# Optimization experiments

Measured on AMD Instinct MI355X. Metric: run time of the kernel, lower is better.

## Reference

```python
import jax, jax.numpy as jnp
import numpy as np

H = W = 240

def setup_inputs() -> dict:
    key = jax.random.key(0)
    k1, k2, k3 = jax.random.split(key, 3)
    B = 256
    T2_Gen = jax.random.normal(k1, (B, 1, H, W), dtype=jnp.float32)
    underT2_K = jax.random.normal(k2, (B, 2, H, W), dtype=jnp.float32)
    # k-space sampling mask (soft in [0,1); original uses a fixed undersampling mask)
    A = jax.random.uniform(k3, (H, W), dtype=jnp.float32)
    return {"T2_Gen": T2_Gen, "underT2_K": underT2_K, "A": A}

def reference(T2_Gen, underT2_K, A):
    # x2: [B, H, W]
    x2 = T2_Gen.reshape(-1, H, W)
    # batched 2D FFT over the last two axes (replaces the per-slice numpy loop)
    x2_k = jnp.fft.fft2(x2)  # complex64
    # undersampled k-space as complex: real = channel 0, imag = channel 1
    y_k = underT2_K[:, 0, :, :] + 1j * underT2_K[:, 1, :, :]
    z_k = (1.0 - A) * x2_k + y_k
    z = jnp.abs(jnp.fft.ifft2(z_k))  # [B, H, W] real
    return z.reshape(-1, 1, H, W)
```

## Files before the change

kernel.cpp:

```cpp
#include <hip/hip_runtime.h>
#include <hip/hip_fp16.h>
#include <math.h>

#define HW 240
#define PITCH 242
#define IMG_PIX (HW*HW)
#define NB 15
#define NBA 8
#define TILE_ELEMS (240*16)
#define CHA 4
#define CHC 3

__device__ __forceinline__ float2 cmul(float2 a, float2 b){
    return make_float2(a.x*b.x - a.y*b.y, a.x*b.y + a.y*b.x);
}
__device__ __forceinline__ float2 cadd(float2 a, float2 b){
    return make_float2(a.x+b.x, a.y+b.y);
}
__device__ __forceinline__ float2 csub(float2 a, float2 b){
    return make_float2(a.x-b.x, a.y-b.y);
}
__device__ __forceinline__ __half2 f2h(float2 a){ return __floats2half2_rn(a.x, a.y); }
__device__ __forceinline__ float2 h2f(__half2 h){ return make_float2(__low2float(h), __high2float(h)); }

__device__ __forceinline__ void wave_fence(){ __builtin_amdgcn_wave_barrier(); }

__device__ __forceinline__ void lds_barrier(){
    asm volatile("s_waitcnt lgkmcnt(0)" ::: "memory");
    __builtin_amdgcn_s_barrier();
    asm volatile("" ::: "memory");
}

template<int SIGN>
__device__ __forceinline__ void dft15(const float2* x, float2* X){
    const float S = (float)SIGN;
    const float s3 = 0.8660254037844387f;
    float2 y[5][3];
    #pragma unroll
    for (int n2 = 0; n2 < 5; ++n2){
        float2 a0 = x[n2], a1 = x[5+n2], a2 = x[10+n2];
        float2 t = cadd(a1, a2);
        float2 u = csub(a1, a2);
        float2 m = make_float2(a0.x - 0.5f*t.x, a0.y - 0.5f*t.y);
        float sx = S * s3;
        float2 s = make_float2(-sx*u.y, sx*u.x);
        y[n2][0] = cadd(a0, t);
        y[n2][1] = cadd(m, s);
        y[n2][2] = csub(m, s);
    }
    const float C15[9] = {1.f, 0.9135454576426009f, 0.6691306063588582f, 0.30901699437494745f,
                          -0.10452846326765346f, -0.5f, -0.8090169943749475f,
                          -0.9781476007338057f, -0.9781476007338057f};
    const float S15[9] = {0.f, 0.4067366430758004f, 0.7431448254773942f, 0.9510565162951535f,
                          0.9945218953682733f, 0.8660254037844387f, 0.5877852522924731f,
                          0.20791169081775931f, -0.20791169081775931f};
    #pragma unroll
    for (int n2 = 1; n2 < 5; ++n2){
        #pragma unroll
        for (int k1 = 1; k1 < 3; ++k1){
            const int e = n2*k1;
            y[n2][k1] = cmul(y[n2][k1], make_float2(C15[e], S*S15[e]));
        }
    }
    const float c1 = 0.30901699437494745f, s1 = 0.9510565162951535f;
    const float c2 = -0.8090169943749475f, s2 = 0.5877852522924731f;
    #pragma unroll
    for (int k1 = 0; k1 < 3; ++k1){
        float2 x0 = y[0][k1], x1 = y[1][k1], x2 = y[2][k1], x3 = y[3][k1], x4 = y[4][k1];
        float2 t1 = cadd(x1, x4), t3 = csub(x1, x4);
        float2 t2 = cadd(x2, x3), t4 = csub(x2, x3);
        X[k1] = make_float2(x0.x + t1.x + t2.x, x0.y + t1.y + t2.y);
        float2 u1 = make_float2(x0.x + c1*t1.x + c2*t2.x, x0.y + c1*t1.y + c2*t2.y);
        float2 u2 = make_float2(x0.x + c2*t1.x + c1*t2.x, x0.y + c2*t1.y + c1*t2.y);
        float2 v1 = make_float2(S*(s1*t3.x + s2*t4.x), S*(s1*t3.y + s2*t4.y));
        float2 v2 = make_float2(S*(s2*t3.x - s1*t4.x), S*(s2*t3.y - s1*t4.y));
        X[k1+3]  = make_float2(u1.x - v1.y, u1.y + v1.x);
        X[k1+12] = make_float2(u1.x + v1.y, u1.y - v1.x);
        X[k1+6]  = make_float2(u2.x - v2.y, u2.y + v2.x);
        X[k1+9]  = make_float2(u2.x + v2.y, u2.y - v2.x);
    }
}

template<int SIGN>
__device__ __forceinline__ void dft16(const float2* x, float2* X){
    const float S = (float)SIGN;
    float2 y[4][4];
    #pragma unroll
    for (int n2 = 0; n2 < 4; ++n2){
        float2 a0 = x[n2], a1 = x[4+n2], a2 = x[8+n2], a3 = x[12+n2];
        float2 t0 = cadd(a0,a2), t1 = csub(a0,a2);
        float2 t2 = cadd(a1,a3), t3 = csub(a1,a3);
        float2 it3 = make_float2(-S*t3.y, S*t3.x);
        y[n2][0] = cadd(t0,t2);
        y[n2][2] = csub(t0,t2);
        y[n2][1] = cadd(t1,it3);
        y[n2][3] = csub(t1,it3);
    }
    const float C16[10] = {1.f, 0.9238795325112867f, 0.7071067811865476f, 0.3826834323650898f,
                           0.f, -0.3826834323650898f, -0.7071067811865476f, -0.9238795325112867f,
                           -1.f, -0.9238795325112867f};
    const float S16[10] = {0.f, 0.3826834323650898f, 0.7071067811865476f, 0.9238795325112867f,
                           1.f, 0.9238795325112867f, 0.7071067811865476f, 0.3826834323650898f,
                           0.f, -0.3826834323650898f};
    #pragma unroll
    for (int n2 = 1; n2 < 4; ++n2){
        #pragma unroll
        for (int k1 = 1; k1 < 4; ++k1){
            const int e = n2*k1;
            y[n2][k1] = cmul(y[n2][k1], make_float2(C16[e], S*S16[e]));
        }
    }
    #pragma unroll
    for (int k1 = 0; k1 < 4; ++k1){
        float2 a0 = y[0][k1], a1 = y[1][k1], a2 = y[2][k1], a3 = y[3][k1];
        float2 t0 = cadd(a0,a2), t1 = csub(a0,a2);
        float2 t2 = cadd(a1,a3), t3 = csub(a1,a3);
        float2 it3 = make_float2(-S*t3.y, S*t3.x);
        X[k1]    = cadd(t0,t2);
        X[k1+8]  = csub(t0,t2);
        X[k1+4]  = cadd(t1,it3);
        X[k1+12] = csub(t1,it3);
    }
}

template<int SIGN>
__device__ __forceinline__ void fft240_core(float2 (*sm)[PITCH], float2* v,
                                            float2* XX, int rl, int b){
    const float TWOPI = 6.28318530717958647692f;
    wave_fence();
    float2 Y[15];
    dft15<SIGN>(v, Y);
    float2 step, tw = make_float2(1.0f, 0.0f);
    {
        float ang = (float)SIGN * TWOPI * (float)b * (1.0f/240.0f);
        __sincosf(ang, &step.y, &step.x);
    }
    #pragma unroll
    for (int d = 0; d < 15; ++d){
        sm[rl][b*15 + d] = cmul(Y[d], tw);
        tw = cmul(tw, step);
    }
    wave_fence();
    float2 Z[16];
    if (b < 15){
        #pragma unroll
        for (int bb = 0; bb < 16; ++bb) Z[bb] = sm[rl][bb*15 + b];
    }
    wave_fence();
    if (b < 15) dft16<SIGN>(Z, XX);
}

template<int SIGN>
__device__ __forceinline__ void fft240(float2 (*sm)[PITCH], float2* v, int rl, int b){
    float2 XX[16];
    fft240_core<SIGN>(sm, v, XX, rl, b);
    if (b < 15){
        #pragma unroll
        for (int m = 0; m < 16; ++m) sm[rl][15*m + b] = XX[m];
    }
    wave_fence();
}

__global__ __launch_bounds__(256) void passA_rowfft(const float* __restrict__ x,
                                                    __half2* __restrict__ out){
    __shared__ __align__(16) float2 sm[15][PITCH];
    int g = blockIdx.x;
    int tid = threadIdx.x, rl = tid >> 4, b = tid & 15;
    if (tid >= 240) return;
    float2 v[15];
    {
        int c = g*CHA; int img = c / NBA, h0 = (c % NBA) * 30;
        const float* r0 = x + (size_t)img * IMG_PIX + (size_t)(h0 + 2*rl) * HW;
        #pragma unroll
        for (int a = 0; a < 15; ++a)
            v[a] = make_float2(r0[16*a + b], r0[HW + 16*a + b]);
    }
    for (int t = 0; t < CHA; ++t){
        int c = g*CHA + t; int img = c / NBA, h0 = (c % NBA) * 30;
        float2 nv[15];
        if (t+1 < CHA){
            int c2 = c + 1; int img2 = c2 / NBA, h02 = (c2 % NBA) * 30;
            const float* r0 = x + (size_t)img2 * IMG_PIX + (size_t)(h02 + 2*rl) * HW;
            #pragma unroll
            for (int a = 0; a < 15; ++a)
                nv[a] = make_float2(r0[16*a + b], r0[HW + 16*a + b]);
        }
        asm volatile("" ::: "memory");
        fft240<-1>(sm, v, rl, b);
        #pragma unroll
        for (int kb = 0; kb < NB; ++kb){
            int k = kb*16 + b;
            int km = k ? 240 - k : 0;
            float2 P = sm[rl][k], Q = sm[rl][km];
            float2 Xa = make_float2(0.5f*(P.x + Q.x), 0.5f*(P.y - Q.y));
            float2 Xb = make_float2(0.5f*(P.y + Q.y), 0.5f*(Q.x - P.x));
            size_t o = ((size_t)(img*NB + kb)*HW + (h0 + 2*rl))*16 + b;
            out[o]      = f2h(Xa);
            out[o + 16] = f2h(Xb);
        }
        if (t+1 < CHA){
            #pragma unroll
            for (int a = 0; a < 15; ++a) v[a] = nv[a];
        }
    }
}

__global__ __launch_bounds__(256) void passB_col_dc_icol(__half2* __restrict__ io,
                                                         const float* __restrict__ under,
                                                         const float* __restrict__ Am){
    __shared__ __align__(16) float2 sm[16][PITCH];
    int g = blockIdx.x, img = g / NB, s = g % NB, kw0 = s * 16;
    int tid = threadIdx.x, rl = tid >> 4, b = tid & 15;
    __half2* chunk = io + (size_t)(img*NB + s) * TILE_ELEMS;

    if (tid < 240){
        #pragma unroll
        for (int jj = 0; jj < 4; ++jj){
            int k = jj*240 + tid;
            float4 raw = *(const float4*)(chunk + 4*k);
            const __half2* hp = (const __half2*)&raw;
            int col = k >> 2;
            int r0 = (4*k) & 15;
            #pragma unroll
            for (int i = 0; i < 4; ++i) sm[r0 + i][col] = h2f(hp[i]);
        }
    }
    const float* y0 = under + (size_t)img * (2*IMG_PIX);
    float y0r[15], y1r[15];
    #pragma unroll
    for (int j = 0; j < 15; ++j){
        size_t p = (size_t)(j*16 + rl) * HW + kw0 + b;
        y0r[j] = y0[p];
        y1r[j] = y0[IMG_PIX + p];
    }
    asm volatile("" ::: "memory");
    lds_barrier();
    float2 v[15];
    #pragma unroll
    for (int a = 0; a < 15; ++a) v[a] = sm[rl][16*a + b];
    float2 XX[16];
    fft240_core<-1>(sm, v, XX, rl, b);
    if (b < 15){
        #pragma unroll
        for (int m = 0; m < 16; ++m) sm[rl][15*m + b] = XX[m];
    }
    lds_barrier();
    #pragma unroll
    for (int j = 0; j < 15; ++j){
        int kh = j*16 + rl;
        size_t p = (size_t)kh * HW + kw0 + b;
        float sc = 1.0f - Am[p];
        float2 X = sm[b][kh];
        sm[b][kh] = make_float2(sc * X.x + y0r[j], sc * X.y + y1r[j]);
    }
    lds_barrier();
    float2 v2[15];
    #pragma unroll
    for (int a = 0; a < 15; ++a) v2[a] = sm[rl][16*a + b];
    float2 ZZ[16];
    fft240_core<+1>(sm, v2, ZZ, rl, b);
    const float inv240 = 1.0f / 240.0f;
    if (b < 15){
        #pragma unroll
        for (int m = 0; m < 16; ++m)
            chunk[(size_t)(15*m + b)*16 + rl] =
                f2h(make_float2(ZZ[m].x*inv240, ZZ[m].y*inv240));
    }
}

__global__ __launch_bounds__(256) void passC_irow_abs(const __half2* __restrict__ in,
                                                      float* __restrict__ outp){
    __shared__ __align__(16) float2 sm[16][PITCH];
    int g = blockIdx.x;
    int tid = threadIdx.x, rl = tid >> 4, b = tid & 15;
    float2 v[15];
    {
        int c = g*CHC; int img = c / NB, h0 = (c % NB) * 16;
        #pragma unroll
        for (int a = 0; a < 15; ++a)
            v[a] = h2f(in[((size_t)(img*NB + a)*HW + h0 + rl)*16 + b]);
    }
    const float inv240 = 1.0f / 240.0f;
    for (int t = 0; t < CHC; ++t){
        int c = g*CHC + t; int img = c / NB, h0 = (c % NB) * 16;
        float2 nv[15];
        if (t+1 < CHC){
            int c2 = c + 1; int img2 = c2 / NB, h02 = (c2 % NB) * 16;
            #pragma unroll
            for (int a = 0; a < 15; ++a)
                nv[a] = h2f(in[((size_t)(img2*NB + a)*HW + h02 + rl)*16 + b]);
        }
        asm volatile("" ::: "memory");
        float2 XX[16];
        fft240_core<+1>(sm, v, XX, rl, b);
        float* dst = outp + (size_t)img * IMG_PIX + (size_t)(h0 + rl) * HW;
        if (b < 15){
            #pragma unroll
            for (int m = 0; m < 16; ++m){
                float2 X = XX[m];
                dst[15*m + b] = sqrtf(X.x*X.x + X.y*X.y) * inv240;
            }
        }
        if (t+1 < CHC){
            #pragma unroll
            for (int a = 0; a < 15; ++a) v[a] = nv[a];
        }
    }
}

extern "C" void kernel_launch(void* const* d_in, const int* in_sizes, int n_in,
                              void* d_out, int out_size, void* d_ws, size_t ws_size,
                              hipStream_t stream){
    const float* T2   = (const float*)d_in[0];
    const float* U    = (const float*)d_in[1];
    const float* Am   = (const float*)d_in[2];
    float* out        = (float*)d_out;

    const int B = 256;
    __half2* i1 = (__half2*)d_ws;

    dim3 block(256);
    passA_rowfft     <<<dim3(B * NBA / CHA), block, 0, stream>>>(T2, i1);
    passB_col_dc_icol<<<dim3(B * NB),        block, 0, stream>>>(i1, U, Am);
    passC_irow_abs   <<<dim3(B * NB / CHC),  block, 0, stream>>>(i1, out);
}
```

Measured before the change: 294.2 us.

## Re-tile intermediate layout so row-FFT writes and column-FFT reads coalesce

Pass A now handles one 16-row strip per block with 128 threads and stages its half-precision spectrum in LDS, so each block writes whole 16-wide tiles with vector stores. Those tiles are laid out so pass B can read its column input directly into registers without an LDS transpose. Pass B now stages its inverse-column result in LDS and writes it back with vector stores in the layout pass C expects. The cross-chunk prefetch and register buffering of the measurement data are dropped, which may expose more load latency.

Measured after the change: 274.1 us. 6.8% less time.

```diff
diff --git a/kernel.cpp b/kernel.cpp
--- a/kernel.cpp
+++ b/kernel.cpp
@@ -6,9 +6,7 @@
 #define PITCH 242
 #define IMG_PIX (HW*HW)
 #define NB 15
-#define NBA 8
 #define TILE_ELEMS (240*16)
-#define CHA 4
 #define CHC 3
 
 __device__ __forceinline__ float2 cmul(float2 a, float2 b){
@@ -161,46 +159,43 @@
     wave_fence();
 }
 
-__global__ __launch_bounds__(256) void passA_rowfft(const float* __restrict__ x,
+
+__global__ __launch_bounds__(128) void passA_rowfft(const float* __restrict__ x,
                                                     __half2* __restrict__ out){
-    __shared__ __align__(16) float2 sm[15][PITCH];
-    int g = blockIdx.x;
+    __shared__ __align__(16) float2 smbuf[8*PITCH];
+    float2 (*sm)[PITCH] = (float2(*)[PITCH])smbuf;
+    __half2* Lh = (__half2*)smbuf;
+    int g = blockIdx.x, img = g / NB, Ag = g % NB, h0 = Ag * 16;
     int tid = threadIdx.x, rl = tid >> 4, b = tid & 15;
-    if (tid >= 240) return;
+    const float* r0 = x + (size_t)img * IMG_PIX + (size_t)(h0 + 2*rl) * HW;
     float2 v[15];
-    {
-        int c = g*CHA; int img = c / NBA, h0 = (c % NBA) * 30;
-        const float* r0 = x + (size_t)img * IMG_PIX + (size_t)(h0 + 2*rl) * HW;
-        #pragma unroll
-        for (int a = 0; a < 15; ++a)
-            v[a] = make_float2(r0[16*a + b], r0[HW + 16*a + b]);
-    }
-    for (int t = 0; t < CHA; ++t){
-        int c = g*CHA + t; int img = c / NBA, h0 = (c % NBA) * 30;
-        float2 nv[15];
-        if (t+1 < CHA){
-            int c2 = c + 1; int img2 = c2 / NBA, h02 = (c2 % NBA) * 30;
-            const float* r0 = x + (size_t)img2 * IMG_PIX + (size_t)(h02 + 2*rl) * HW;
-            #pragma unroll
-            for (int a = 0; a < 15; ++a)
-                nv[a] = make_float2(r0[16*a + b], r0[HW + 16*a + b]);
-        }
-        asm volatile("" ::: "memory");
-        fft240<-1>(sm, v, rl, b);
-        #pragma unroll
-        for (int kb = 0; kb < NB; ++kb){
-            int k = kb*16 + b;
-            int km = k ? 240 - k : 0;
-            float2 P = sm[rl][k], Q = sm[rl][km];
-            float2 Xa = make_float2(0.5f*(P.x + Q.x), 0.5f*(P.y - Q.y));
-            float2 Xb = make_float2(0.5f*(P.y + Q.y), 0.5f*(Q.x - P.x));
-            size_t o = ((size_t)(img*NB + kb)*HW + (h0 + 2*rl))*16 + b;
-            out[o]      = f2h(Xa);
-            out[o + 16] = f2h(Xb);
-        }
-        if (t+1 < CHA){
-            #pragma unroll
-            for (int a = 0; a < 15; ++a) v[a] = nv[a];
+    #pragma unroll
+    for (int a = 0; a < 15; ++a)
+        v[a] = make_float2(r0[16*a + b], r0[HW + 16*a + b]);
+    fft240<-1>(sm, v, rl, b);
+    __half2 xa[15], xb[15];
+    #pragma unroll
+    for (int kb = 0; kb < NB; ++kb){
+        int k = kb*16 + b;
+        int km = k ? 240 - k : 0;
+        float2 P = sm[rl][k], Q = sm[rl][km];
+        xa[kb] = f2h(make_float2(0.5f*(P.x + Q.x), 0.5f*(P.y - Q.y)));
+        xb[kb] = f2h(make_float2(0.5f*(P.y + Q.y), 0.5f*(Q.x - P.x)));
+    }
+    lds_barrier();
+    #pragma unroll
+    for (int kb = 0; kb < NB; ++kb){
+        Lh[kb*256 + b*16 + 2*rl]     = xa[kb];
+        Lh[kb*256 + b*16 + 2*rl + 1] = xb[kb];
+    }
+    lds_barrier();
+    float4* gout = (float4*)out;
+    #pragma unroll
+    for (int i = 0; i < 8; ++i){
+        int u = i*128 + tid;
+        if (u < 960){
+            int seg = u >> 6, e = u & 63;
+            gout[((size_t)(img*NB + seg)*NB + Ag)*64 + e] = ((float4*)Lh)[u];
         }
     }
 }
@@ -213,31 +208,11 @@
     int tid = threadIdx.x, rl = tid >> 4, b = tid & 15;
     __half2* chunk = io + (size_t)(img*NB + s) * TILE_ELEMS;
 
-    if (tid < 240){
-        #pragma unroll
-        for (int jj = 0; jj < 4; ++jj){
-            int k = jj*240 + tid;
-            float4 raw = *(const float4*)(chunk + 4*k);
-            const __half2* hp = (const __half2*)&raw;
-            int col = k >> 2;
-            int r0 = (4*k) & 15;
-            #pragma unroll
-            for (int i = 0; i < 4; ++i) sm[r0 + i][col] = h2f(hp[i]);
-        }
-    }
-    const float* y0 = under + (size_t)img * (2*IMG_PIX);
-    float y0r[15], y1r[15];
-    #pragma unroll
-    for (int j = 0; j < 15; ++j){
-        size_t p = (size_t)(j*16 + rl) * HW + kw0 + b;
-        y0r[j] = y0[p];
-        y1r[j] = y0[IMG_PIX + p];
-    }
-    asm volatile("" ::: "memory");
-    lds_barrier();
     float2 v[15];
     #pragma unroll
-    for (int a = 0; a < 15; ++a) v[a] = sm[rl][16*a + b];
+    for (int a = 0; a < 15; ++a)
+        v[a] = h2f(chunk[a*256 + rl*16 + b]);
+
     float2 XX[16];
     fft240_core<-1>(sm, v, XX, rl, b);
     if (b < 15){
@@ -245,13 +220,14 @@
         for (int m = 0; m < 16; ++m) sm[rl][15*m + b] = XX[m];
     }
     lds_barrier();
+    const float* y0 = under + (size_t)img * (2*IMG_PIX);
     #pragma unroll
     for (int j = 0; j < 15; ++j){
         int kh = j*16 + rl;
         size_t p = (size_t)kh * HW + kw0 + b;
         float sc = 1.0f - Am[p];
         float2 X = sm[b][kh];
-        sm[b][kh] = make_float2(sc * X.x + y0r[j], sc * X.y + y1r[j]);
+        sm[b][kh] = make_float2(sc * X.x + y0[p], sc * X.y + y0[IMG_PIX + p]);
     }
     lds_barrier();
     float2 v2[15];
@@ -263,8 +239,21 @@
     if (b < 15){
         #pragma unroll
         for (int m = 0; m < 16; ++m)
-            chunk[(size_t)(15*m + b)*16 + rl] =
-                f2h(make_float2(ZZ[m].x*inv240, ZZ[m].y*inv240));
+            sm[rl][15*m + b] = make_float2(ZZ[m].x*inv240, ZZ[m].y*inv240);
+    }
+    lds_barrier();
+    if (tid < 240){
+        #pragma unroll
+        for (int jj = 0; jj < 4; ++jj){
+            int k = jj*240 + tid;
+            int col = k >> 2;
+            int r0 = (4*k) & 15;
+            float4 outv;
+            __half2* op = (__half2*)&outv;
+            #pragma unroll
+            for (int i = 0; i < 4; ++i) op[i] = f2h(sm[r0 + i][col]);
+            *(float4*)(chunk + 4*k) = outv;
+        }
     }
 }
 
@@ -319,8 +308,7 @@
     const int B = 256;
     __half2* i1 = (__half2*)d_ws;
 
-    dim3 block(256);
-    passA_rowfft     <<<dim3(B * NBA / CHA), block, 0, stream>>>(T2, i1);
-    passB_col_dc_icol<<<dim3(B * NB),        block, 0, stream>>>(i1, U, Am);
-    passC_irow_abs   <<<dim3(B * NB / CHC),  block, 0, stream>>>(i1, out);
-}
+    passA_rowfft     <<<dim3(B * NB),       dim3(128), 0, stream>>>(T2, i1);
+    passB_col_dc_icol<<<dim3(B * NB),       dim3(256), 0, stream>>>(i1, U, Am);
+    passC_irow_abs   <<<dim3(B * NB / CHC), dim3(256), 0, stream>>>(i1, out);
+}
```
